# Kernel optimization log

Measured on AMD Instinct MI355X. Metric: run time of the kernel, lower is better.

Reference implementation:

```python
import jax, jax.numpy as jnp
import numpy as np

B, S, D, H = 4096, 200, 64, 36
BN_EPS = 1e-5
DICE_EPS = 1e-3


def setup_inputs() -> dict:
    key = jax.random.key(0)
    ks = jax.random.split(key, 6)
    return {
        "history": jax.random.normal(ks[0], (B, S, D), dtype=jnp.float32),
        "candidate": jax.random.normal(ks[1], (B, D), dtype=jnp.float32),
        "W1": jax.random.normal(ks[2], (4 * D, H), dtype=jnp.float32) * 0.05,
        "b1": jax.random.normal(ks[3], (H,), dtype=jnp.float32) * 0.05,
        "gamma": jnp.ones((H,), dtype=jnp.float32),
        "beta": jnp.zeros((H,), dtype=jnp.float32),
        "alpha": jax.random.normal(ks[4], (1,), dtype=jnp.float32),
        "W2": jax.random.normal(ks[5], (H, 1), dtype=jnp.float32) * 0.05,
        "b2": jnp.zeros((1,), dtype=jnp.float32),
    }


def reference(history, candidate, W1, b1, gamma, beta, alpha, W2, b2):
    b, s, d = history.shape
    cand = jnp.broadcast_to(candidate[:, None, :], (b, s, d))
    att_in = jnp.concatenate([cand, history, cand - history, cand * history], axis=-1)
    x = att_in.reshape(b * s, 4 * d)
    # Linear
    h = x @ W1 + b1
    # BatchNorm1d (training mode: batch statistics, biased variance)
    mu = h.mean(axis=0)
    var = h.var(axis=0)
    h = (h - mu) * jax.lax.rsqrt(var + BN_EPS) * gamma + beta
    # Dice: per-row normalization over features, eps=1e-3
    avg = h.mean(axis=1, keepdims=True)
    v = jnp.sum((h - avg) ** 2, axis=1, keepdims=True) / h.shape[1]
    ps = jax.nn.sigmoid((h - avg) / jnp.sqrt(v + DICE_EPS))
    h = ps * h + (1.0 - ps) * alpha * h
    # Output linear -> attention weight per (b, s)
    w = (h @ W2 + b2).reshape(b, s)
    # Weighted sum pooling over sequence
    return jnp.einsum("bs,bsd->bd", w, history)
```

## Files before the change

### kernel.cpp

```cpp
#include <hip/hip_runtime.h>
#include <hip/hip_bf16.h>
#include <math.h>

#define BB 4096
#define SS 200
#define DD 64
#define HH 36
#define NP 48
#define NTI 13
#define NROWSF (4096.0f * 200.0f)
#define PSTRIDE 80

typedef short bf16x8 __attribute__((ext_vector_type(8)));
typedef float f32x4 __attribute__((ext_vector_type(4)));

__device__ __forceinline__ unsigned short f2bf(float f) {
    union { float f; unsigned u; } v; v.f = f;
    unsigned r = v.u + 0x7FFFu + ((v.u >> 16) & 1u);
    return (unsigned short)(r >> 16);
}
__device__ __forceinline__ unsigned f2bf2(float a, float b) {
    union { __hip_bfloat162 h; unsigned u; } v;
    v.h = __float22bfloat162_rn(float2{a, b});
    return v.u;
}

__device__ __forceinline__ void gl_lds16(const void* g, void* l) {
    __builtin_amdgcn_global_load_lds(
        (const __attribute__((address_space(1))) unsigned*)g,
        (__attribute__((address_space(3))) unsigned*)l, 16, 0, 0);
}

__global__ __launch_bounds__(256) void k_wb(const float* __restrict__ cand,
                                            const float* __restrict__ W1,
                                            const float* __restrict__ b1,
                                            unsigned short* __restrict__ WbG,
                                            float* __restrict__ baseG) {
    int b = blockIdx.x, t = threadIdx.x;
    __shared__ float shC[DD];
    if (t < DD) shC[t] = cand[b * DD + t];
    __syncthreads();
    unsigned short* wb = WbG + (size_t)b * (NP * DD);
#pragma unroll
    for (int u = 0; u < 12; ++u) {
        int e = t + u * 256;
        int n = e >> 6, k = e & 63;
        float val = 0.f;
        if (n < HH)
            val = W1[(DD + k) * HH + n] - W1[(2 * DD + k) * HH + n] +
                  shC[k] * W1[(3 * DD + k) * HH + n];
        wb[e] = f2bf(val);
    }
    if (t < NP) {
        float v = 0.f;
        if (t < HH) {
            v = b1[t];
            for (int k = 0; k < DD; ++k)
                v += shC[k] * (W1[k * HH + t] + W1[(2 * DD + k) * HH + t]);
        }
        baseG[b * NP + t] = v;
    }
}

template <bool WB>
__device__ __forceinline__ void prologue512(int b, int t,
                                            const float* __restrict__ hist,
                                            const float* __restrict__ cand,
                                            const float* __restrict__ W1,
                                            const float* __restrict__ b1,
                                            const unsigned short* __restrict__ WbG,
                                            const float* __restrict__ baseG,
                                            float* shHf, unsigned short* shWbT,
                                            float* shC, float* shBase,
                                            float (*shBaseP)[NP]) {
    const float* hsrc = hist + (size_t)b * SS * DD;
    if (WB) {
        const char* hb = (const char*)hsrc;
        char* lb = (char*)shHf;
#pragma unroll
        for (int j = 0; j < 6; ++j)
            gl_lds16(hb + (j * 512 + t) * 16, lb + (j * 512 + t) * 16);
        if (t < 128) gl_lds16(hb + (3072 + t) * 16, lb + (3072 + t) * 16);
        const char* wbsrc = (const char*)(WbG + (size_t)b * (NP * DD));
        if (t < 384) gl_lds16(wbsrc + t * 16, (char*)shWbT + t * 16);
        if (t < NP) shBase[t] = baseG[b * NP + t];
        if (t < 128)
            *(float4*)&shHf[SS * DD + t * 4] = float4{0.f, 0.f, 0.f, 0.f};
        __syncthreads();
    } else {
        if (t < DD) shC[t] = cand[b * DD + t];
        const float4* src = (const float4*)hsrc;
        float4 v[7];
#pragma unroll
        for (int u = 0; u < 6; ++u) v[u] = src[t + u * 512];
        if (t < 128) v[6] = src[t + 3072];
        if (t < 128)
            *(float4*)&shHf[SS * DD + t * 4] = float4{0.f, 0.f, 0.f, 0.f};
        __syncthreads();
#pragma unroll
        for (int u = 0; u < 6; ++u) *(float4*)&shHf[(t + u * 512) * 4] = v[u];
        if (t < 128) *(float4*)&shHf[(t + 3072) * 4] = v[6];
        for (int e = t; e < NP * DD; e += 512) {
            int n = e >> 6, k = e & 63;
            float val = 0.f;
            if (n < HH)
                val = W1[(DD + k) * HH + n] - W1[(2 * DD + k) * HH + n] +
                      shC[k] * W1[(3 * DD + k) * HH + n];
            shWbT[n * DD + k] = f2bf(val);
        }
        if (t < 4 * NP) {
            int g = t / NP, j = t - g * NP;
            float p = 0.f;
            if (j < HH) {
#pragma unroll 4
                for (int k = 16 * g; k < 16 * g + 16; ++k)
                    p += shC[k] * (W1[k * HH + j] + W1[(2 * DD + k) * HH + j]);
            }
            shBaseP[g][j] = p;
        }
        __syncthreads();
        if (t < NP) {
            float val = (t < HH) ? b1[t] : 0.f;
            shBase[t] = val + shBaseP[0][t] + shBaseP[1][t] + shBaseP[2][t] +
                        shBaseP[3][t];
        }
        __syncthreads();
    }
}

__device__ __forceinline__ void load_bfrags(const unsigned short* shWbT, int lane,
                                            bf16x8 (&bfr)[3][2]) {
    int col = lane & 15, q = lane >> 4;
#pragma unroll
    for (int nt = 0; nt < 3; ++nt)
#pragma unroll
        for (int kt = 0; kt < 2; ++kt)
            bfr[nt][kt] = *(const bf16x8*)&shWbT[(nt * 16 + col) * DD + kt * 32 + q * 8];
}

__device__ __forceinline__ bf16x8 load_afrag(const float* shHf, int m, int kt, int q) {
    const float* rp = shHf + m * DD + kt * 32 + q * 8;
    f32x4 x0 = *(const f32x4*)rp;
    f32x4 x1 = *(const f32x4*)(rp + 4);
    union { bf16x8 b8; unsigned u[4]; } a;
    a.u[0] = f2bf2(x0[0], x0[1]);
    a.u[1] = f2bf2(x0[2], x0[3]);
    a.u[2] = f2bf2(x1[0], x1[1]);
    a.u[3] = f2bf2(x1[2], x1[3]);
    return a.b8;
}

__device__ __forceinline__ void gemm_tile(const float* shHf,
                                          const bf16x8 (&bfr)[3][2], int mt, int lane,
                                          f32x4 (&d)[3]) {
    int m = mt * 16 + (lane & 15), q = lane >> 4;
    d[0] = f32x4{0.f, 0.f, 0.f, 0.f};
    d[1] = f32x4{0.f, 0.f, 0.f, 0.f};
    d[2] = f32x4{0.f, 0.f, 0.f, 0.f};
#pragma unroll
    for (int kt = 0; kt < 2; ++kt) {
        bf16x8 a = load_afrag(shHf, m, kt, q);
#pragma unroll
        for (int nt = 0; nt < 3; ++nt)
            d[nt] = __builtin_amdgcn_mfma_f32_16x16x32_bf16(a, bfr[nt][kt], d[nt], 0, 0, 0);
    }
}

template <bool WB, bool RED>
__global__ __launch_bounds__(512, 4) void k_pass1(const float* __restrict__ hist,
                                                  const float* __restrict__ cand,
                                                  const float* __restrict__ W1,
                                                  const float* __restrict__ b1,
                                                  const unsigned short* __restrict__ WbG,
                                                  const float* __restrict__ baseG,
                                                  float* __restrict__ pstat,
                                                  float* __restrict__ gsum,
                                                  float* __restrict__ gsum2) {
    __shared__ __align__(16) float shHf[(SS + 8) * DD];
    __shared__ __align__(16) unsigned short shWbT[NP * DD];
    __shared__ float shC[WB ? 1 : DD], shBase[NP];
    __shared__ float shBaseP[WB ? 1 : 4][NP];
    __shared__ float shP1[8][NP], shP2[8][NP];
    int b = blockIdx.x;
    int t = threadIdx.x, wave = t >> 6, lane = t & 63;
    int col = lane & 15, q = lane >> 4;

    prologue512<WB>(b, t, hist, cand, W1, b1, WbG, baseG, shHf, shWbT, shC,
                    shBase, shBaseP);

    bf16x8 bfr[3][2];
    load_bfrags(shWbT, lane, bfr);
    float basev[3];
#pragma unroll
    for (int nt = 0; nt < 3; ++nt) basev[nt] = shBase[nt * 16 + col];

    float cs1[3] = {0.f, 0.f, 0.f}, cs2[3] = {0.f, 0.f, 0.f};
    for (int mt = wave; mt < NTI; mt += 8) {
        f32x4 d[3];
        gemm_tile(shHf, bfr, mt, lane, d);
        if (mt == 12) {
            int grow0 = 192 + q * 4;
#pragma unroll
            for (int nt = 0; nt < 3; ++nt)
#pragma unroll
                for (int r = 0; r < 4; ++r)
                    if (grow0 + r < SS) {
                        float vv = d[nt][r] + basev[nt];
                        cs1[nt] += vv;
                        cs2[nt] += vv * vv;
                    }
        } else {
#pragma unroll
            for (int nt = 0; nt < 3; ++nt)
#pragma unroll
                for (int r = 0; r < 4; ++r) {
                    float vv = d[nt][r] + basev[nt];
                    cs1[nt] += vv;
                    cs2[nt] += vv * vv;
                }
        }
    }
#pragma unroll
    for (int nt = 0; nt < 3; ++nt) {
        cs1[nt] += __shfl_xor(cs1[nt], 16);
        cs1[nt] += __shfl_xor(cs1[nt], 32);
        cs2[nt] += __shfl_xor(cs2[nt], 16);
        cs2[nt] += __shfl_xor(cs2[nt], 32);
    }
    if (lane < 16) {
#pragma unroll
        for (int nt = 0; nt < 3; ++nt) {
            shP1[wave][nt * 16 + lane] = cs1[nt];
            shP2[wave][nt * 16 + lane] = cs2[nt];
        }
    }
    __syncthreads();
    if (RED) {
        if (t < HH) {
            float s = 0.f;
#pragma unroll
            for (int w = 0; w < 8; ++w) s += shP1[w][t];
            pstat[(size_t)b * PSTRIDE + t] = s;
        } else if (t < 2 * HH) {
            int f = t - HH;
            float s = 0.f;
#pragma unroll
            for (int w = 0; w < 8; ++w) s += shP2[w][f];
            pstat[(size_t)b * PSTRIDE + t] = s;
        }
    } else {
        if (t < HH) {
            float s1 = 0.f, s2 = 0.f;
#pragma unroll
            for (int w = 0; w < 8; ++w) { s1 += shP1[w][t]; s2 += shP2[w][t]; }
            atomicAdd(gsum + t, s1);
            atomicAdd(gsum2 + t, s2);
        }
    }
}

__global__ __launch_bounds__(256) void k_stats_red(const float* __restrict__ pstat,
                                                   const float* __restrict__ gamma,
                                                   const float* __restrict__ beta,
                                                   float* __restrict__ A,
                                                   float* __restrict__ Bc) {
    int f = blockIdx.x, t = threadIdx.x;
    if (f >= HH) {
        if (t == 0) { A[f] = 0.f; Bc[f] = 0.f; }
        return;
    }
    float s1 = 0.f, s2 = 0.f;
    for (int r = t; r < BB; r += 256) {
        s1 += pstat[(size_t)r * PSTRIDE + f];
        s2 += pstat[(size_t)r * PSTRIDE + HH + f];
    }
#pragma unroll
    for (int off = 1; off < 64; off <<= 1) {
        s1 += __shfl_xor(s1, off);
        s2 += __shfl_xor(s2, off);
    }
    __shared__ float a1[4], a2[4];
    if ((t & 63) == 0) { a1[t >> 6] = s1; a2[t >> 6] = s2; }
    __syncthreads();
    if (t == 0) {
        s1 = a1[0] + a1[1] + a1[2] + a1[3];
        s2 = a2[0] + a2[1] + a2[2] + a2[3];
        float mu = s1 * (1.0f / NROWSF);
        float var = s2 * (1.0f / NROWSF) - mu * mu;
        float a = rsqrtf(var + 1e-5f) * gamma[f];
        A[f] = a;
        Bc[f] = beta[f] - mu * a;
    }
}

__global__ void k_stats(const float* __restrict__ gsum, const float* __restrict__ gsum2,
                        const float* __restrict__ gamma, const float* __restrict__ beta,
                        float* __restrict__ A, float* __restrict__ Bc) {
    int t = threadIdx.x;
    if (t < NP) {
        if (t < HH) {
            float mu = gsum[t] * (1.0f / NROWSF);
            float var = gsum2[t] * (1.0f / NROWSF) - mu * mu;
            float a = rsqrtf(var + 1e-5f) * gamma[t];
            A[t] = a;
            Bc[t] = beta[t] - mu * a;
        } else {
            A[t] = 0.f;
            Bc[t] = 0.f;
        }
    }
}

template <bool WB>
__global__ __launch_bounds__(512, 4) void k_pass2(const float* __restrict__ hist,
                                                  const float* __restrict__ cand,
                                                  const float* __restrict__ W1,
                                                  const float* __restrict__ b1,
                                                  const unsigned short* __restrict__ WbG,
                                                  const float* __restrict__ baseG,
                                                  const float* __restrict__ Acoef,
                                                  const float* __restrict__ Bcoef,
                                                  const float* __restrict__ alpha,
                                                  const float* __restrict__ W2,
                                                  const float* __restrict__ b2,
                                                  float* __restrict__ out) {
    __shared__ __align__(16) float shHf[(SS + 8) * DD];
    __shared__ __align__(16) unsigned short shWbT[NP * DD];
    __shared__ float shC[WB ? 1 : DD], shBase[NP];
    __shared__ float shBaseP[WB ? 1 : 4][NP];
    __shared__ float shW[(SS + 8)];
    __shared__ float shPool[8][DD];
    int b = blockIdx.x;
    int t = threadIdx.x, wave = t >> 6, lane = t & 63;
    int col = lane & 15, q = lane >> 4;

    prologue512<WB>(b, t, hist, cand, W1, b1, WbG, baseG, shHf, shWbT, shC,
                    shBase, shBaseP);

    bf16x8 bfr[3][2];
    load_bfrags(shWbT, lane, bfr);
    float baseAB[3], Ar[3], W2r[3];
#pragma unroll
    for (int nt = 0; nt < 3; ++nt) {
        int c = nt * 16 + col;
        Ar[nt] = Acoef[c];
        baseAB[nt] = fmaf(shBase[c], Ar[nt], Bcoef[c]);
        W2r[nt] = (c < HH) ? W2[c] : 0.f;
    }
    float alv = alpha[0], one_m_alv = 1.0f - alv, b2v = b2[0];

    for (int mt = wave; mt < NTI; mt += 8) {
        f32x4 d[3];
        gemm_tile(shHf, bfr, mt, lane, d);
        float hp[3][4];
#pragma unroll
        for (int nt = 0; nt < 3; ++nt)
#pragma unroll
            for (int r = 0; r < 4; ++r)
                hp[nt][r] = fmaf(d[nt][r], Ar[nt], baseAB[nt]);
        float s1[4], s2[4], wsum[4];
#pragma unroll
        for (int r = 0; r < 4; ++r) {
            s1[r] = hp[0][r] + hp[1][r] + hp[2][r];
            s2[r] = hp[0][r] * hp[0][r] + hp[1][r] * hp[1][r] + hp[2][r] * hp[2][r];
            s1[r] += __shfl_xor(s1[r], 1);
            s1[r] += __shfl_xor(s1[r], 2);
            s1[r] += __shfl_xor(s1[r], 4);
            s1[r] += __shfl_xor(s1[r], 8);
            s2[r] += __shfl_xor(s2[r], 1);
            s2[r] += __shfl_xor(s2[r], 2);
            s2[r] += __shfl_xor(s2[r], 4);
            s2[r] += __shfl_xor(s2[r], 8);
        }
#pragma unroll
        for (int r = 0; r < 4; ++r) {
            float avg = s1[r] * (1.0f / (float)HH);
            float var = s2[r] * (1.0f / (float)HH) - avg * avg;
            float inv = rsqrtf(var + 1e-3f);
            float wv = 0.f;
#pragma unroll
            for (int nt = 0; nt < 3; ++nt) {
                float z = (hp[nt][r] - avg) * inv;
                float ps = 1.0f / (1.0f + __expf(-z));
                float f = fmaf(ps, one_m_alv, alv);
                wv = fmaf(hp[nt][r] * f, W2r[nt], wv);
            }
            wsum[r] = wv;
            wsum[r] += __shfl_xor(wsum[r], 1);
            wsum[r] += __shfl_xor(wsum[r], 2);
            wsum[r] += __shfl_xor(wsum[r], 4);
            wsum[r] += __shfl_xor(wsum[r], 8);
        }
        if (col == 0) {
            float4 o = {wsum[0] + b2v, wsum[1] + b2v, wsum[2] + b2v, wsum[3] + b2v};
            *(float4*)&shW[mt * 16 + q * 4] = o;
        }
    }
    __syncthreads();
    {
        float p = 0.f;
        for (int s = wave; s < SS; s += 8)
            p = fmaf(shW[s], shHf[s * DD + lane], p);
        shPool[wave][lane] = p;
    }
    __syncthreads();
    if (t < DD) {
        float s = 0.f;
#pragma unroll
        for (int w = 0; w < 8; ++w) s += shPool[w][t];
        out[b * DD + t] = s;
    }
}

extern "C" void kernel_launch(void* const* d_in, const int* in_sizes, int n_in,
                              void* d_out, int out_size, void* d_ws, size_t ws_size,
                              hipStream_t stream) {
    const float* hist = (const float*)d_in[0];
    const float* cand = (const float*)d_in[1];
    const float* W1 = (const float*)d_in[2];
    const float* b1 = (const float*)d_in[3];
    const float* gamma = (const float*)d_in[4];
    const float* beta = (const float*)d_in[5];
    const float* alpha = (const float*)d_in[6];
    const float* W2 = (const float*)d_in[7];
    const float* b2 = (const float*)d_in[8];
    float* out = (float*)d_out;
    float* ws = (float*)d_ws;

    const size_t pstatF = (size_t)BB * PSTRIDE;
    const size_t baseF = (size_t)BB * NP;
    const size_t wbBytes = (size_t)BB * NP * DD * 2;
    const size_t fullNeed = (pstatF + 2 * NP + baseF) * 4 + wbBytes;
    const size_t midNeed = (pstatF + 2 * NP) * 4;

    if (ws_size >= fullNeed) {
        float* pstat = ws;
        float* A = pstat + pstatF;
        float* Bc = A + NP;
        float* baseG = Bc + NP;
        unsigned short* WbG = (unsigned short*)(baseG + baseF);
        k_wb<<<BB, 256, 0, stream>>>(cand, W1, b1, WbG, baseG);
        k_pass1<true, true><<<BB, 512, 0, stream>>>(hist, cand, W1, b1, WbG, baseG,
                                                    pstat, nullptr, nullptr);
        k_stats_red<<<NP, 256, 0, stream>>>(pstat, gamma, beta, A, Bc);
        k_pass2<true><<<BB, 512, 0, stream>>>(hist, cand, W1, b1, WbG, baseG, A, Bc,
                                              alpha, W2, b2, out);
    } else if (ws_size >= midNeed) {
        float* pstat = ws;
        float* A = pstat + pstatF;
        float* Bc = A + NP;
        k_pass1<false, true><<<BB, 512, 0, stream>>>(hist, cand, W1, b1, nullptr,
                                                     nullptr, pstat, nullptr, nullptr);
        k_stats_red<<<NP, 256, 0, stream>>>(pstat, gamma, beta, A, Bc);
        k_pass2<false><<<BB, 512, 0, stream>>>(hist, cand, W1, b1, nullptr, nullptr,
                                               A, Bc, alpha, W2, b2, out);
    } else {
        float* gsum = ws;
        float* gsum2 = ws + NP;
        float* A = ws + 2 * NP;
        float* Bc = ws + 3 * NP;
        hipMemsetAsync(gsum, 0, 2 * NP * sizeof(float), stream);
        k_pass1<false, false><<<BB, 512, 0, stream>>>(hist, cand, W1, b1, nullptr,
                                                      nullptr, nullptr, gsum, gsum2);
        k_stats<<<1, 64, 0, stream>>>(gsum, gsum2, gamma, beta, A, Bc);
        k_pass2<false><<<BB, 512, 0, stream>>>(hist, cand, W1, b1, nullptr, nullptr,
                                               A, Bc, alpha, W2, b2, out);
    }
}
```

Before: 418.5 us.

## Drop precomputed per-batch weight kernel; compute folded weights in-prologue overlapped with async history load

New measurement: 485.2 us. 15.9% more time.

```diff
diff --git a/kernel.cpp b/kernel.cpp
--- a/kernel.cpp
+++ b/kernel.cpp
@@ -31,101 +31,46 @@
         (__attribute__((address_space(3))) unsigned*)l, 16, 0, 0);
 }
 
-__global__ __launch_bounds__(256) void k_wb(const float* __restrict__ cand,
-                                            const float* __restrict__ W1,
-                                            const float* __restrict__ b1,
-                                            unsigned short* __restrict__ WbG,
-                                            float* __restrict__ baseG) {
-    int b = blockIdx.x, t = threadIdx.x;
-    __shared__ float shC[DD];
-    if (t < DD) shC[t] = cand[b * DD + t];
-    __syncthreads();
-    unsigned short* wb = WbG + (size_t)b * (NP * DD);
-#pragma unroll
-    for (int u = 0; u < 12; ++u) {
-        int e = t + u * 256;
-        int n = e >> 6, k = e & 63;
-        float val = 0.f;
-        if (n < HH)
-            val = W1[(DD + k) * HH + n] - W1[(2 * DD + k) * HH + n] +
-                  shC[k] * W1[(3 * DD + k) * HH + n];
-        wb[e] = f2bf(val);
-    }
-    if (t < NP) {
-        float v = 0.f;
-        if (t < HH) {
-            v = b1[t];
-            for (int k = 0; k < DD; ++k)
-                v += shC[k] * (W1[k * HH + t] + W1[(2 * DD + k) * HH + t]);
-        }
-        baseG[b * NP + t] = v;
-    }
-}
-
-template <bool WB>
 __device__ __forceinline__ void prologue512(int b, int t,
                                             const float* __restrict__ hist,
                                             const float* __restrict__ cand,
                                             const float* __restrict__ W1,
                                             const float* __restrict__ b1,
-                                            const unsigned short* __restrict__ WbG,
-                                            const float* __restrict__ baseG,
                                             float* shHf, unsigned short* shWbT,
-                                            float* shC, float* shBase,
-                                            float (*shBaseP)[NP]) {
+                                            float* shBase) {
     const float* hsrc = hist + (size_t)b * SS * DD;
-    if (WB) {
-        const char* hb = (const char*)hsrc;
-        char* lb = (char*)shHf;
-#pragma unroll
-        for (int j = 0; j < 6; ++j)
-            gl_lds16(hb + (j * 512 + t) * 16, lb + (j * 512 + t) * 16);
-        if (t < 128) gl_lds16(hb + (3072 + t) * 16, lb + (3072 + t) * 16);
-        const char* wbsrc = (const char*)(WbG + (size_t)b * (NP * DD));
-        if (t < 384) gl_lds16(wbsrc + t * 16, (char*)shWbT + t * 16);
-        if (t < NP) shBase[t] = baseG[b * NP + t];
-        if (t < 128)
-            *(float4*)&shHf[SS * DD + t * 4] = float4{0.f, 0.f, 0.f, 0.f};
-        __syncthreads();
-    } else {
-        if (t < DD) shC[t] = cand[b * DD + t];
-        const float4* src = (const float4*)hsrc;
-        float4 v[7];
-#pragma unroll
-        for (int u = 0; u < 6; ++u) v[u] = src[t + u * 512];
-        if (t < 128) v[6] = src[t + 3072];
-        if (t < 128)
-            *(float4*)&shHf[SS * DD + t * 4] = float4{0.f, 0.f, 0.f, 0.f};
-        __syncthreads();
-#pragma unroll
-        for (int u = 0; u < 6; ++u) *(float4*)&shHf[(t + u * 512) * 4] = v[u];
-        if (t < 128) *(float4*)&shHf[(t + 3072) * 4] = v[6];
-        for (int e = t; e < NP * DD; e += 512) {
-            int n = e >> 6, k = e & 63;
-            float val = 0.f;
-            if (n < HH)
-                val = W1[(DD + k) * HH + n] - W1[(2 * DD + k) * HH + n] +
-                      shC[k] * W1[(3 * DD + k) * HH + n];
-            shWbT[n * DD + k] = f2bf(val);
-        }
-        if (t < 4 * NP) {
-            int g = t / NP, j = t - g * NP;
-            float p = 0.f;
-            if (j < HH) {
-#pragma unroll 4
-                for (int k = 16 * g; k < 16 * g + 16; ++k)
-                    p += shC[k] * (W1[k * HH + j] + W1[(2 * DD + k) * HH + j]);
-            }
-            shBaseP[g][j] = p;
-        }
-        __syncthreads();
-        if (t < NP) {
-            float val = (t < HH) ? b1[t] : 0.f;
-            shBase[t] = val + shBaseP[0][t] + shBaseP[1][t] + shBaseP[2][t] +
-                        shBaseP[3][t];
-        }
-        __syncthreads();
-    }
+    const char* hb = (const char*)hsrc;
+    char* lb = (char*)shHf;
+#pragma unroll
+    for (int j = 0; j < 6; ++j)
+        gl_lds16(hb + (j * 512 + t) * 16, lb + (j * 512 + t) * 16);
+    if (t < 128) gl_lds16(hb + (3072 + t) * 16, lb + (3072 + t) * 16);
+    if (t < 128)
+        *(float4*)&shHf[SS * DD + t * 4] = float4{0.f, 0.f, 0.f, 0.f};
+
+    const float* c = cand + b * DD;
+    float ck = c[t & 63];
+#pragma unroll
+    for (int u = 0; u < 6; ++u) {
+        int e = t + u * 512;
+        int n = e >> 6, k = e & 63;
+        float val = 0.f;
+        if (n < HH)
+            val = W1[(DD + k) * HH + n] - W1[(2 * DD + k) * HH + n] +
+                  ck * W1[(3 * DD + k) * HH + n];
+        shWbT[n * DD + k] = f2bf(val);
+    }
+    if (t < NP) {
+        float v = 0.f;
+        if (t < HH) {
+            v = b1[t];
+#pragma unroll 8
+            for (int k = 0; k < DD; ++k)
+                v += c[k] * (W1[k * HH + t] + W1[(2 * DD + k) * HH + t]);
+        }
+        shBase[t] = v;
+    }
+    __syncthreads();
 }
 
 __device__ __forceinline__ void load_bfrags(const unsigned short* shWbT, int lane,
@@ -166,27 +111,23 @@
     }
 }
 
-template <bool WB, bool RED>
+template <bool RED>
 __global__ __launch_bounds__(512, 4) void k_pass1(const float* __restrict__ hist,
                                                   const float* __restrict__ cand,
                                                   const float* __restrict__ W1,
                                                   const float* __restrict__ b1,
-                                                  const unsigned short* __restrict__ WbG,
-                                                  const float* __restrict__ baseG,
                                                   float* __restrict__ pstat,
                                                   float* __restrict__ gsum,
                                                   float* __restrict__ gsum2) {
     __shared__ __align__(16) float shHf[(SS + 8) * DD];
     __shared__ __align__(16) unsigned short shWbT[NP * DD];
-    __shared__ float shC[WB ? 1 : DD], shBase[NP];
-    __shared__ float shBaseP[WB ? 1 : 4][NP];
+    __shared__ float shBase[NP];
     __shared__ float shP1[8][NP], shP2[8][NP];
     int b = blockIdx.x;
     int t = threadIdx.x, wave = t >> 6, lane = t & 63;
     int col = lane & 15, q = lane >> 4;
 
-    prologue512<WB>(b, t, hist, cand, W1, b1, WbG, baseG, shHf, shWbT, shC,
-                    shBase, shBaseP);
+    prologue512(b, t, hist, cand, W1, b1, shHf, shWbT, shBase);
 
     bf16x8 bfr[3][2];
     load_bfrags(shWbT, lane, bfr);
@@ -311,13 +252,10 @@
     }
 }
 
-template <bool WB>
 __global__ __launch_bounds__(512, 4) void k_pass2(const float* __restrict__ hist,
                                                   const float* __restrict__ cand,
                                                   const float* __restrict__ W1,
                                                   const float* __restrict__ b1,
-                                                  const unsigned short* __restrict__ WbG,
-                                                  const float* __restrict__ baseG,
                                                   const float* __restrict__ Acoef,
                                                   const float* __restrict__ Bcoef,
                                                   const float* __restrict__ alpha,
@@ -326,16 +264,14 @@
                                                   float* __restrict__ out) {
     __shared__ __align__(16) float shHf[(SS + 8) * DD];
     __shared__ __align__(16) unsigned short shWbT[NP * DD];
-    __shared__ float shC[WB ? 1 : DD], shBase[NP];
-    __shared__ float shBaseP[WB ? 1 : 4][NP];
+    __shared__ float shBase[NP];
     __shared__ float shW[(SS + 8)];
     __shared__ float shPool[8][DD];
     int b = blockIdx.x;
     int t = threadIdx.x, wave = t >> 6, lane = t & 63;
     int col = lane & 15, q = lane >> 4;
 
-    prologue512<WB>(b, t, hist, cand, W1, b1, WbG, baseG, shHf, shWbT, shC,
-                    shBase, shBaseP);
+    prologue512(b, t, hist, cand, W1, b1, shHf, shWbT, shBase);
 
     bf16x8 bfr[3][2];
     load_bfrags(shWbT, lane, bfr);
@@ -428,42 +364,27 @@
     float* ws = (float*)d_ws;
 
     const size_t pstatF = (size_t)BB * PSTRIDE;
-    const size_t baseF = (size_t)BB * NP;
-    const size_t wbBytes = (size_t)BB * NP * DD * 2;
-    const size_t fullNeed = (pstatF + 2 * NP + baseF) * 4 + wbBytes;
     const size_t midNeed = (pstatF + 2 * NP) * 4;
 
-    if (ws_size >= fullNeed) {
+    if (ws_size >= midNeed) {
         float* pstat = ws;
         float* A = pstat + pstatF;
         float* Bc = A + NP;
-        float* baseG = Bc + NP;
-        unsigned short* WbG = (unsigned short*)(baseG + baseF);
-        k_wb<<<BB, 256, 0, stream>>>(cand, W1, b1, WbG, baseG);
-        k_pass1<true, true><<<BB, 512, 0, stream>>>(hist, cand, W1, b1, WbG, baseG,
-                                                    pstat, nullptr, nullptr);
+        k_pass1<true><<<BB, 512, 0, stream>>>(hist, cand, W1, b1, pstat, nullptr,
+                                              nullptr);
         k_stats_red<<<NP, 256, 0, stream>>>(pstat, gamma, beta, A, Bc);
-        k_pass2<true><<<BB, 512, 0, stream>>>(hist, cand, W1, b1, WbG, baseG, A, Bc,
-                                              alpha, W2, b2, out);
-    } else if (ws_size >= midNeed) {
-        float* pstat = ws;
-        float* A = pstat + pstatF;
-        float* Bc = A + NP;
-        k_pass1<false, true><<<BB, 512, 0, stream>>>(hist, cand, W1, b1, nullptr,
-                                                     nullptr, pstat, nullptr, nullptr);
-        k_stats_red<<<NP, 256, 0, stream>>>(pstat, gamma, beta, A, Bc);
-        k_pass2<false><<<BB, 512, 0, stream>>>(hist, cand, W1, b1, nullptr, nullptr,
-                                               A, Bc, alpha, W2, b2, out);
+        k_pass2<<<BB, 512, 0, stream>>>(hist, cand, W1, b1, A, Bc, alpha, W2, b2,
+                                        out);
     } else {
         float* gsum = ws;
         float* gsum2 = ws + NP;
         float* A = ws + 2 * NP;
         float* Bc = ws + 3 * NP;
         hipMemsetAsync(gsum, 0, 2 * NP * sizeof(float), stream);
-        k_pass1<false, false><<<BB, 512, 0, stream>>>(hist, cand, W1, b1, nullptr,
-                                                      nullptr, nullptr, gsum, gsum2);
+        k_pass1<false><<<BB, 512, 0, stream>>>(hist, cand, W1, b1, nullptr, gsum,
+                                               gsum2);
         k_stats<<<1, 64, 0, stream>>>(gsum, gsum2, gamma, beta, A, Bc);
-        k_pass2<false><<<BB, 512, 0, stream>>>(hist, cand, W1, b1, nullptr, nullptr,
-                                               A, Bc, alpha, W2, b2, out);
-    }
-}
+        k_pass2<<<BB, 512, 0, stream>>>(hist, cand, W1, b1, A, Bc, alpha, W2, b2,
+                                        out);
+    }
+}
```
